# Kernel tuning notes

Measured on AMD Instinct MI355X. Metric: run time of the kernel, lower is better.

The kernel has to match this reference:

```python
import jax, jax.numpy as jnp
import numpy as np

# Static problem sizes
B, TMAX = 32, 48                 # subjects, max windows per subject
NPW, NWIN = 128, 1024            # nodes per window, total windows (= sum(lengths))
EPW = 2048                       # edges per window (avg degree 16)
N, E = NWIN * NPW, NWIN * EPW    # 131072 nodes, 2097152 edges
IN_DIM, GNN_H, GRU_H = 128, 128, 128


def setup_inputs() -> dict:
    key = jax.random.key(0)
    ks = jax.random.split(key, 12)
    x = jax.random.normal(ks[0], (N, IN_DIM), jnp.float32)
    # random intra-window edges: endpoints within each window's 128-node block
    base = jax.random.randint(ks[1], (2, NWIN, EPW), 0, NPW)
    offs = (jnp.arange(NWIN) * NPW)[None, :, None]
    edge_index = (base + offs).reshape(2, E)
    batch_idx = jnp.repeat(jnp.arange(NWIN), NPW)          # node -> window id
    lengths = jnp.asarray(np.tile([16, 48], B // 2), jnp.int32)  # sums to NWIN
    s = 0.05
    p = lambda k, shape: jax.random.normal(k, shape, jnp.float32) * s
    return dict(
        x=x, edge_index=edge_index, batch_idx=batch_idx, lengths=lengths,
        # GIN layer 1 MLP (weights stored [in,out])
        w1a=p(ks[2], (IN_DIM, GNN_H)), b1a=jnp.zeros((GNN_H,), jnp.float32),
        w1b=p(ks[3], (GNN_H, GNN_H)), b1b=jnp.zeros((GNN_H,), jnp.float32),
        # GIN layer 2 MLP
        w2a=p(ks[4], (GNN_H, GNN_H)), b2a=jnp.zeros((GNN_H,), jnp.float32),
        w2b=p(ks[5], (GNN_H, GNN_H)), b2b=jnp.zeros((GNN_H,), jnp.float32),
        # GRU (torch layout: [3H, in], gate order r,z,n)
        wih=p(ks[6], (3 * GRU_H, GNN_H)), whh=p(ks[7], (3 * GRU_H, GRU_H)),
        bih=jnp.zeros((3 * GRU_H,), jnp.float32), bhh=jnp.zeros((3 * GRU_H,), jnp.float32),
        # output head
        wout=p(ks[8], (GRU_H, 1)), bout=jnp.zeros((1,), jnp.float32),
    )


def _gin(h, src, dst, wa, ba, wb, bb):
    # GINConv with eps=0: mlp(x + sum_{j->i} x_j)
    aggr = jax.ops.segment_sum(h[src], dst, num_segments=N)
    z = h + aggr
    z = jax.nn.relu(z @ wa + ba)
    return z @ wb + bb


def _forward(x, w1a, b1a, w1b, b1b, w2a, b2a, w2b, b2b,
             wih, whh, bih, bhh, wout, bout, edge_index, batch_idx, lengths):
    src, dst = edge_index[0], edge_index[1]
    h = jax.nn.relu(_gin(x, src, dst, w1a, b1a, w1b, b1b))
    h = jax.nn.relu(_gin(h, src, dst, w2a, b2a, w2b, b2b))
    # global mean pool per window -> [NWIN, GNN_H]
    sums = jax.ops.segment_sum(h, batch_idx, num_segments=NWIN)
    cnt = jax.ops.segment_sum(jnp.ones((N, 1), h.dtype), batch_idx, num_segments=NWIN)
    g = sums / cnt
    # pad_sequence: scatter flat window embeddings into [B, TMAX, H]
    csum = jnp.cumsum(lengths)
    starts = jnp.concatenate([jnp.zeros((1,), lengths.dtype), csum[:-1]])
    win_ids = jnp.arange(NWIN)
    subj = jnp.searchsorted(csum, win_ids, side='right')
    pos = win_ids - starts[subj]
    padded = jnp.zeros((B, TMAX, GNN_H), g.dtype).at[subj, pos].set(g)
    # masked GRU == pack_padded_sequence semantics (state frozen past length)
    mask = jnp.arange(TMAX)[:, None] < lengths[None, :]   # [T, B]
    xs = jnp.swapaxes(padded, 0, 1)                        # [T, B, H]

    def step(hc, inputs):
        xt, mt = inputs
        gx = xt @ wih.T + bih
        gh = hc @ whh.T + bhh
        rx, zx, nx = jnp.split(gx, 3, axis=-1)
        rh, zh, nh = jnp.split(gh, 3, axis=-1)
        r = jax.nn.sigmoid(rx + rh)
        z = jax.nn.sigmoid(zx + zh)
        n = jnp.tanh(nx + r * nh)
        hn = (1 - z) * n + z * hc
        hn = jnp.where(mt[:, None], hn, hc)
        return hn, None

    h0 = jnp.zeros((B, GRU_H), g.dtype)
    h_last, _ = jax.lax.scan(step, h0, (xs, mask))
    return (h_last @ wout + bout).squeeze(-1)  # [B]


def reference(x, edge_index, batch_idx, lengths,
              w1a, b1a, w1b, b1b, w2a, b2a, w2b, b2b,
              wih, whh, bih, bhh, wout, bout):
    return _forward(x, w1a, b1a, w1b, b1b, w2a, b2a, w2b, b2b,
                    wih, whh, bih, bhh, wout, bout, edge_index, batch_idx, lengths)
```

## Files before the change

### kernel.cpp

```cpp
#include <hip/hip_runtime.h>
#include <hip/hip_bf16.h>
#include <stdint.h>

#define NPW   128
#define NWIN  1024
#define EPW   2048
#define NEDGE (NWIN * EPW)
#define BSUBJ 32
#define TMAXW 48

typedef __bf16 bf16x8_t __attribute__((ext_vector_type(8)));
typedef float  f32x4_t  __attribute__((ext_vector_type(4)));

#define MU4_OFF  0
#define B2_OFF   8192
#define B3_OFF   40960
#define BIAS_OFF 73728
#define GP_OFF   75776
#define META_OFF 76288
#define K1_LDS   76800

__device__ __forceinline__ unsigned short bfbits(float v) {
  return __builtin_bit_cast(unsigned short, (__bf16)v);
}

#define GLDS16(gaddr, laddr) __builtin_amdgcn_global_load_lds( \
    (const __attribute__((address_space(1))) unsigned*)(gaddr), \
    (__attribute__((address_space(3))) unsigned*)(laddr), 16, 0, 0)

__device__ __forceinline__ void wstage(const char* src, char* dstB3, int wv, int lane) {
  #pragma unroll
  for (int p = 0; p < 4; ++p)
    GLDS16(src + wv * 4096 + p * 1024 + lane * 16, dstB3 + wv * 4096 + p * 1024);
}

__device__ __forceinline__ void gemm_lds(const char* Ab, const char* Bb, int lane, int rt,
                                         f32x4_t acc[8]) {
  const int rowA = rt * 16 + (lane & 15);
  const int swA = (rowA & 15) << 4;
  const int swB = (lane & 15) << 4;
  #pragma unroll
  for (int kk = 0; kk < 4; ++kk) {
    const int kb = kk * 64 + (lane >> 4) * 16;
    bf16x8_t af = *(const bf16x8_t*)(Ab + rowA * 256 + (kb ^ swA));
    #pragma unroll
    for (int ct = 0; ct < 8; ++ct) {
      const int rowB = ct * 16 + (lane & 15);
      bf16x8_t bv = *(const bf16x8_t*)(Bb + rowB * 256 + (kb ^ swB));
      acc[ct] = __builtin_amdgcn_mfma_f32_16x16x32_bf16(af, bv, acc[ct], 0, 0, 0);
    }
  }
}

__device__ __forceinline__ void gemm_m(const unsigned* Mw, const char* Bb, int lane, int rt,
                                       f32x4_t acc[8]) {
  const int rowA = rt * 16 + (lane & 15);
  const int g = lane >> 4;
  const int swB = (lane & 15) << 4;
  #pragma unroll
  for (int kk = 0; kk < 4; ++kk) {
    const unsigned mw = Mw[rowA * 16 + ((kk * 4 + g) ^ (rowA & 15))];
    bf16x8_t af;
    #pragma unroll
    for (int e = 0; e < 8; ++e)
      af[e] = (__bf16)(float)((mw >> (4 * e)) & 15u);
    const int kb = kk * 64 + g * 16;
    #pragma unroll
    for (int ct = 0; ct < 8; ++ct) {
      const int rowB = ct * 16 + (lane & 15);
      bf16x8_t bv = *(const bf16x8_t*)(Bb + rowB * 256 + (kb ^ swB));
      acc[ct] = __builtin_amdgcn_mfma_f32_16x16x32_bf16(af, bv, acc[ct], 0, 0, 0);
    }
  }
}

__device__ __forceinline__ void write_row(char* Dst, int lane, int rt, const f32x4_t acc[8],
                                          const float* bias, bool relu) {
  const int r0 = rt * 16 + (lane >> 4) * 4;
  const int c = lane & 15;
  #pragma unroll
  for (int ct = 0; ct < 8; ++ct) {
    const int col = ct * 16 + c;
    const float bvl = bias ? bias[col] : 0.f;
    #pragma unroll
    for (int j = 0; j < 4; ++j) {
      float v = acc[ct][j] + bvl;
      if (relu) v = fmaxf(v, 0.f);
      const int row = r0 + j;
      *(__bf16*)(Dst + row * 256 + ((col * 2) ^ ((row & 15) << 4))) = (__bf16)v;
    }
  }
}

__device__ __forceinline__ void write_tr(char* Dst, int lane, int rt, const f32x4_t acc[8]) {
  const int r0 = rt * 16 + (lane >> 4) * 4;
  const int c = lane & 15;
  #pragma unroll
  for (int ct = 0; ct < 8; ++ct) {
    const int col = ct * 16 + c;
    unsigned long long pk = 0ull;
    #pragma unroll
    for (int j = 0; j < 4; ++j)
      pk |= ((unsigned long long)bfbits(acc[ct][j])) << (16 * j);
    *(unsigned long long*)(Dst + col * 256 + ((r0 * 2) ^ ((col & 15) << 4))) = pk;
  }
}

__global__ void __launch_bounds__(128)
wprep_kernel(const float* __restrict__ w1a, const float* __restrict__ w1b,
             const float* __restrict__ w2a, const float* __restrict__ w2b,
             unsigned* __restrict__ wt) {
  const float* srcs[4] = {w1a, w1b, w2a, w2b};
  const float* src = srcs[blockIdx.x];
  const int j = threadIdx.x;
  unsigned* dst = wt + blockIdx.x * 8192 + j * 64;
  const int sw = (j & 15) << 2;
  #pragma unroll 8
  for (int k = 0; k < 64; ++k) {
    float a = src[(size_t)(2 * k) * 128 + j];
    float b = src[(size_t)(2 * k + 1) * 128 + j];
    dst[k ^ sw] = (unsigned)bfbits(a) | ((unsigned)bfbits(b) << 16);
  }
}

__global__ void __launch_bounds__(512, 2)
gin_gnn_kernel(const float* __restrict__ x, const int* __restrict__ ei,
               const float* __restrict__ b1a, const float* __restrict__ b1b,
               const float* __restrict__ b2a, const float* __restrict__ b2b,
               const char* __restrict__ wt_sw, const float* __restrict__ wih,
               const float* __restrict__ bih, const int* __restrict__ lengths,
               float* __restrict__ GX) {
  extern __shared__ __align__(16) char sm[];
  const int w = blockIdx.x;
  const int tid = threadIdx.x;
  const int lane = tid & 63;
  const int wv = tid >> 6;

  unsigned* Mw = (unsigned*)(sm + MU4_OFF);
  char* B2 = sm + B2_OFF;
  char* B3 = sm + B3_OFF;
  float* biasb = (float*)(sm + BIAS_OFF);
  float* gp = (float*)(sm + GP_OFF);
  int* meta = (int*)(sm + META_OFF);

  #pragma unroll
  for (int i = tid; i < 2048; i += 512) Mw[i] = 0u;
  if (tid < 128) gp[tid] = 0.f;
  __syncthreads();

  wstage(wt_sw, B3, wv, lane);
  if (tid < 64) {
    int L = (tid < BSUBJ) ? lengths[tid] : 0;
    int c = L;
    #pragma unroll
    for (int d = 1; d < 32; d <<= 1) {
      int u = __shfl_up(c, d, 64);
      if (tid >= d) c += u;
    }
    unsigned long long mset = __ballot(tid < BSUBJ && w < c);
    int s = (int)(__ffsll((long long)mset) - 1);
    if (tid == s) { meta[0] = s; meta[1] = w - (c - L); }
  }
  {
    const int base = w * EPW;
    #pragma unroll
    for (int rr = 0; rr < 4; ++rr) {
      const int e = base + tid + rr * 512;
      const int s = ei[e] & 127;
      const int d = ei[NEDGE + e] & 127;
      atomicAdd(&Mw[d * 16 + ((s >> 3) ^ (d & 15))], 1u << ((s & 7) * 4));
    }
    if (tid < 128) {
      const int d = tid;
      atomicAdd(&Mw[d * 16 + ((d >> 3) ^ (d & 15))], 1u << ((d & 7) * 4));
    }
  }
  {
    const float* xw = x + (size_t)w * 16384;
    #pragma unroll
    for (int it = 0; it < 8; ++it) {
      const int elem = it * 2048 + tid * 4;
      const float4 v = *(const float4*)(xw + elem);
      const int row = elem >> 7;
      const int colb = (elem & 127) * 2;
      unsigned long long pk = (unsigned long long)bfbits(v.x)
          | ((unsigned long long)bfbits(v.y) << 16)
          | ((unsigned long long)bfbits(v.z) << 32)
          | ((unsigned long long)bfbits(v.w) << 48);
      *(unsigned long long*)(B2 + row * 256 + (colb ^ ((row & 15) << 4))) = pk;
    }
  }
  {
    const float* bp = (tid < 128) ? b1a : (tid < 256) ? b1b : (tid < 384) ? b2a : b2b;
    biasb[tid] = bp[tid & 127];
  }
  __syncthreads();

  f32x4_t acc[8];
  #define ZACC() { _Pragma("unroll") for (int q = 0; q < 8; ++q) acc[q] = (f32x4_t){0.f,0.f,0.f,0.f}; }

  ZACC(); gemm_lds(B2, B3, lane, wv, acc);
  __syncthreads();
  write_tr(B2, lane, wv, acc);
  wstage(wt_sw + 32768, B3, wv, lane);
  __syncthreads();
  ZACC(); gemm_m(Mw, B2, lane, wv, acc);
  __syncthreads();
  write_row(B2, lane, wv, acc, biasb + 0, true);
  ZACC(); gemm_lds(B2, B3, lane, wv, acc);
  __syncthreads();
  write_row(B2, lane, wv, acc, biasb + 128, true);
  wstage(wt_sw + 65536, B3, wv, lane);
  __syncthreads();
  ZACC(); gemm_lds(B2, B3, lane, wv, acc);
  __syncthreads();
  write_tr(B2, lane, wv, acc);
  wstage(wt_sw + 98304, B3, wv, lane);
  __syncthreads();
  ZACC(); gemm_m(Mw, B2, lane, wv, acc);
  __syncthreads();
  write_row(B2, lane, wv, acc, biasb + 256, true);
  ZACC(); gemm_lds(B2, B3, lane, wv, acc);
  {
    const int c = lane & 15;
    #pragma unroll
    for (int ct = 0; ct < 8; ++ct) {
      const int col = ct * 16 + c;
      const float bvl = biasb[384 + col];
      float s = 0.f;
      #pragma unroll
      for (int j = 0; j < 4; ++j) s += fmaxf(acc[ct][j] + bvl, 0.f);
      s += __shfl_xor(s, 16);
      s += __shfl_xor(s, 32);
      if (lane < 16) atomicAdd(&gp[col], s);
    }
  }
  __syncthreads();

  if (tid < 384) {
    const float* wrow = wih + (size_t)tid * 128;
    const float4* gp4 = (const float4*)gp;
    float a0 = 0.f, a1 = 0.f, a2 = 0.f, a3 = 0.f;
    #pragma unroll
    for (int q = 0; q < 8; ++q) {
      const float4 h0 = gp4[4*q], h1 = gp4[4*q+1], h2 = gp4[4*q+2], h3 = gp4[4*q+3];
      const float4 w0 = *(const float4*)(wrow + 16*q);
      const float4 w1 = *(const float4*)(wrow + 16*q + 4);
      const float4 w2 = *(const float4*)(wrow + 16*q + 8);
      const float4 w3 = *(const float4*)(wrow + 16*q + 12);
      a0 = fmaf(w0.x,h0.x,fmaf(w0.y,h0.y,fmaf(w0.z,h0.z,fmaf(w0.w,h0.w,a0))));
      a1 = fmaf(w1.x,h1.x,fmaf(w1.y,h1.y,fmaf(w1.z,h1.z,fmaf(w1.w,h1.w,a1))));
      a2 = fmaf(w2.x,h2.x,fmaf(w2.y,h2.y,fmaf(w2.z,h2.z,fmaf(w2.w,h2.w,a2))));
      a3 = fmaf(w3.x,h3.x,fmaf(w3.y,h3.y,fmaf(w3.z,h3.z,fmaf(w3.w,h3.w,a3))));
    }
    const float dot = (a0 + a1) + (a2 + a3);
    GX[((size_t)meta[0] * TMAXW + meta[1]) * 384 + tid] = dot * (1.f / 128.f) + bih[tid];
  }
}

#define RL(v, l) __builtin_bit_cast(float, __builtin_amdgcn_readlane(__builtin_bit_cast(int, (v)), (l)))

__global__ void __launch_bounds__(384)
gru_kernel(const float* __restrict__ GX, const float* __restrict__ whh,
           const float* __restrict__ bhh, const float* __restrict__ wout,
           const float* __restrict__ bout, const int* __restrict__ lengths,
           float* __restrict__ outp) {
  __shared__ __align__(8) float hb[128];
  __shared__ float rb[128], zb[128];
  const int b = blockIdx.x;
  const int o = threadIdx.x;
  const int lane = o & 63;

  float wrf[128];
  {
    const float* wr = whh + (size_t)o * 128;
    #pragma unroll
    for (int q = 0; q < 32; ++q) {
      float4 v = ((const float4*)wr)[q];
      wrf[4*q+0] = v.x; wrf[4*q+1] = v.y; wrf[4*q+2] = v.z; wrf[4*q+3] = v.w;
    }
  }
  if (o < 128) hb[o] = 0.f;
  const float bho = bhh[o];
  const int len = lengths[b];
  __syncthreads();

  float2 hv = make_float2(0.f, 0.f);
  float gx = (len > 0) ? GX[((size_t)b * TMAXW) * 384 + o] : 0.f;
  for (int t = 0; t < len; ++t) {
    const int tn = (t + 1 < len) ? t + 1 : t;
    const float gxn = GX[((size_t)b * TMAXW + tn) * 384 + o];
    float a0 = 0.f, a1 = 0.f, a2 = 0.f, a3 = 0.f;
    #pragma unroll
    for (int l4 = 0; l4 < 16; ++l4) {
      const int l0 = 4*l4, l1 = 4*l4+1, l2 = 4*l4+2, l3 = 4*l4+3;
      a0 = fmaf(wrf[2*l0],   RL(hv.x, l0), a0);
      a0 = fmaf(wrf[2*l0+1], RL(hv.y, l0), a0);
      a1 = fmaf(wrf[2*l1],   RL(hv.x, l1), a1);
      a1 = fmaf(wrf[2*l1+1], RL(hv.y, l1), a1);
      a2 = fmaf(wrf[2*l2],   RL(hv.x, l2), a2);
      a2 = fmaf(wrf[2*l2+1], RL(hv.y, l2), a2);
      a3 = fmaf(wrf[2*l3],   RL(hv.x, l3), a3);
      a3 = fmaf(wrf[2*l3+1], RL(hv.y, l3), a3);
    }
    const float gh = (a0 + a1) + (a2 + a3) + bho;
    if (o < 256) {
      const float v = 1.f / (1.f + __expf(-(gx + gh)));
      if (o < 128) rb[o] = v; else zb[o - 128] = v;
    }
    __syncthreads();
    if (o >= 256) {
      const int oo = o - 256;
      const float r = rb[oo], z = zb[oo];
      const float pre = gx + r * gh;
      const float e2 = __expf(-2.f * pre);
      const float n = (1.f - e2) / (1.f + e2);
      hb[oo] = (1.f - z) * n + z * hb[oo];
    }
    __syncthreads();
    hv = *(const float2*)(hb + 2 * lane);
    gx = gxn;
  }

  float part = (o < 128) ? hb[o] * wout[o] : 0.f;
  #pragma unroll
  for (int d = 1; d < 64; d <<= 1) part += __shfl_xor(part, d);
  __shared__ float red[6];
  if ((o & 63) == 0) red[o >> 6] = part;
  __syncthreads();
  if (o == 0) outp[b] = red[0] + red[1] + bout[0];
}

extern "C" void kernel_launch(void* const* d_in, const int* in_sizes, int n_in,
                              void* d_out, int out_size, void* d_ws, size_t ws_size,
                              hipStream_t stream) {
  const float* x    = (const float*)d_in[0];
  const int*   ei   = (const int*)d_in[1];
  const int*   len  = (const int*)d_in[3];
  const float* w1a  = (const float*)d_in[4];
  const float* b1a  = (const float*)d_in[5];
  const float* w1b  = (const float*)d_in[6];
  const float* b1b  = (const float*)d_in[7];
  const float* w2a  = (const float*)d_in[8];
  const float* b2a  = (const float*)d_in[9];
  const float* w2b  = (const float*)d_in[10];
  const float* b2b  = (const float*)d_in[11];
  const float* wih  = (const float*)d_in[12];
  const float* whh  = (const float*)d_in[13];
  const float* bih  = (const float*)d_in[14];
  const float* bhh  = (const float*)d_in[15];
  const float* wout = (const float*)d_in[16];
  const float* bout = (const float*)d_in[17];

  float*    GX    = (float*)d_ws;
  unsigned* wt_sw = (unsigned*)((char*)d_ws + (size_t)BSUBJ * TMAXW * 384 * 4);

  hipLaunchKernelGGL(wprep_kernel, dim3(4), dim3(128), 0, stream,
                     w1a, w1b, w2a, w2b, wt_sw);
  hipLaunchKernelGGL(gin_gnn_kernel, dim3(NWIN), dim3(512), K1_LDS, stream,
                     x, ei, b1a, b1b, b2a, b2b, (const char*)wt_sw,
                     wih, bih, len, GX);
  hipLaunchKernelGGL(gru_kernel, dim3(BSUBJ), dim3(384), 0, stream,
                     GX, whh, bhh, wout, bout, len, (float*)d_out);
}
```

Before: 251.6 us.

## Double-buffer weights and activations in LDS to remove block barriers

```diff
diff --git a/kernel.cpp b/kernel.cpp
--- a/kernel.cpp
+++ b/kernel.cpp
@@ -13,12 +13,14 @@
 typedef float  f32x4_t  __attribute__((ext_vector_type(4)));
 
 #define MU4_OFF  0
-#define B2_OFF   8192
-#define B3_OFF   40960
-#define BIAS_OFF 73728
-#define GP_OFF   75776
-#define META_OFF 76288
-#define K1_LDS   76800
+#define BUFA_OFF 8192
+#define BUFB_OFF 40960
+#define WS1_OFF  73728
+#define WS2_OFF  106496
+#define BIAS_OFF 139264
+#define GP_OFF   141312
+#define META_OFF 141824
+#define K1_LDS   141840
 
 __device__ __forceinline__ unsigned short bfbits(float v) {
   return __builtin_bit_cast(unsigned short, (__bf16)v);
@@ -28,10 +30,10 @@
     (const __attribute__((address_space(1))) unsigned*)(gaddr), \
     (__attribute__((address_space(3))) unsigned*)(laddr), 16, 0, 0)
 
-__device__ __forceinline__ void wstage(const char* src, char* dstB3, int wv, int lane) {
+__device__ __forceinline__ void wstage(const char* src, char* dst, int wv, int lane) {
   #pragma unroll
   for (int p = 0; p < 4; ++p)
-    GLDS16(src + wv * 4096 + p * 1024 + lane * 16, dstB3 + wv * 4096 + p * 1024);
+    GLDS16(src + wv * 4096 + p * 1024 + lane * 16, dst + wv * 4096 + p * 1024);
 }
 
 __device__ __forceinline__ void gemm_lds(const char* Ab, const char* Bb, int lane, int rt,
@@ -137,8 +139,10 @@
   const int wv = tid >> 6;
 
   unsigned* Mw = (unsigned*)(sm + MU4_OFF);
-  char* B2 = sm + B2_OFF;
-  char* B3 = sm + B3_OFF;
+  char* BUFA = sm + BUFA_OFF;
+  char* BUFB = sm + BUFB_OFF;
+  char* WS1 = sm + WS1_OFF;
+  char* WS2 = sm + WS2_OFF;
   float* biasb = (float*)(sm + BIAS_OFF);
   float* gp = (float*)(sm + GP_OFF);
   int* meta = (int*)(sm + META_OFF);
@@ -148,7 +152,8 @@
   if (tid < 128) gp[tid] = 0.f;
   __syncthreads();
 
-  wstage(wt_sw, B3, wv, lane);
+  wstage(wt_sw, WS1, wv, lane);
+  wstage(wt_sw + 32768, WS2, wv, lane);
   if (tid < 64) {
     int L = (tid < BSUBJ) ? lengths[tid] : 0;
     int c = L;
@@ -187,7 +192,7 @@
           | ((unsigned long long)bfbits(v.y) << 16)
           | ((unsigned long long)bfbits(v.z) << 32)
           | ((unsigned long long)bfbits(v.w) << 48);
-      *(unsigned long long*)(B2 + row * 256 + (colb ^ ((row & 15) << 4))) = pk;
+      *(unsigned long long*)(BUFA + row * 256 + (colb ^ ((row & 15) << 4))) = pk;
     }
   }
   {
@@ -199,28 +204,25 @@
   f32x4_t acc[8];
   #define ZACC() { _Pragma("unroll") for (int q = 0; q < 8; ++q) acc[q] = (f32x4_t){0.f,0.f,0.f,0.f}; }
 
-  ZACC(); gemm_lds(B2, B3, lane, wv, acc);
-  __syncthreads();
-  write_tr(B2, lane, wv, acc);
-  wstage(wt_sw + 32768, B3, wv, lane);
-  __syncthreads();
-  ZACC(); gemm_m(Mw, B2, lane, wv, acc);
-  __syncthreads();
-  write_row(B2, lane, wv, acc, biasb + 0, true);
-  ZACC(); gemm_lds(B2, B3, lane, wv, acc);
-  __syncthreads();
-  write_row(B2, lane, wv, acc, biasb + 128, true);
-  wstage(wt_sw + 65536, B3, wv, lane);
-  __syncthreads();
-  ZACC(); gemm_lds(B2, B3, lane, wv, acc);
-  __syncthreads();
-  write_tr(B2, lane, wv, acc);
-  wstage(wt_sw + 98304, B3, wv, lane);
-  __syncthreads();
-  ZACC(); gemm_m(Mw, B2, lane, wv, acc);
-  __syncthreads();
-  write_row(B2, lane, wv, acc, biasb + 256, true);
-  ZACC(); gemm_lds(B2, B3, lane, wv, acc);
+  ZACC(); gemm_lds(BUFA, WS1, lane, wv, acc);
+  write_tr(BUFB, lane, wv, acc);
+  __syncthreads();
+  wstage(wt_sw + 65536, WS1, wv, lane);
+
+  ZACC(); gemm_m(Mw, BUFB, lane, wv, acc);
+  write_row(BUFA, lane, wv, acc, biasb + 0, true);
+  ZACC(); gemm_lds(BUFA, WS2, lane, wv, acc);
+  write_row(BUFA, lane, wv, acc, biasb + 128, true);
+  __syncthreads();
+  wstage(wt_sw + 98304, WS2, wv, lane);
+
+  ZACC(); gemm_lds(BUFA, WS1, lane, wv, acc);
+  write_tr(BUFB, lane, wv, acc);
+  __syncthreads();
+
+  ZACC(); gemm_m(Mw, BUFB, lane, wv, acc);
+  write_row(BUFA, lane, wv, acc, biasb + 256, true);
+  ZACC(); gemm_lds(BUFA, WS2, lane, wv, acc);
   {
     const int c = lane & 15;
     #pragma unroll
@@ -355,6 +357,11 @@
   float*    GX    = (float*)d_ws;
   unsigned* wt_sw = (unsigned*)((char*)d_ws + (size_t)BSUBJ * TMAXW * 384 * 4);
 
+  static bool attr_set = false;
+  (void)attr_set;
+  hipFuncSetAttribute((const void*)gin_gnn_kernel,
+                      hipFuncAttributeMaxDynamicSharedMemorySize, K1_LDS);
+
   hipLaunchKernelGGL(wprep_kernel, dim3(4), dim3(128), 0, stream,
                      w1a, w1b, w2a, w2b, wt_sw);
   hipLaunchKernelGGL(gin_gnn_kernel, dim3(NWIN), dim3(512), K1_LDS, stream,
```

Result: slower. 272.2 us (+8.2%).
